# Performance work log

Hardware: AMD Instinct MI355X
Metric: run time of the kernel (lower is better)

The kernel has to match this reference:

```python
import jax, jax.numpy as jnp
import numpy as np

# Kronecker-sparse patterns (a,b,c,d), rightmost factor first, matching KSLinear.
PATTERNS = ((1, 64, 64, 64), (64, 64, 64, 1))
IN_SIZE = PATTERNS[0][0] * PATTERNS[0][2] * PATTERNS[0][3]   # 4096
OUT_SIZE = PATTERNS[-1][0] * PATTERNS[-1][1] * PATTERNS[-1][3]  # 4096
N_TOKENS = 16384


def setup_inputs() -> dict:
    key = jax.random.key(0)
    kx, k0, k1, kb = jax.random.split(key, 4)
    x = jax.random.normal(kx, (N_TOKENS, IN_SIZE), dtype=jnp.float32)
    # factors stored in native 4D (a,b,c,d) layout, uniform(-1/sqrt(c), 1/sqrt(c))
    a, b, c, d = PATTERNS[0]
    s0 = 1.0 / np.sqrt(c)
    f0 = jax.random.uniform(k0, (a, b, c, d), jnp.float32, -s0, s0)
    a, b, c, d = PATTERNS[1]
    s1 = 1.0 / np.sqrt(c)
    f1 = jax.random.uniform(k1, (a, b, c, d), jnp.float32, -s1, s1)
    bound = 1.0 / np.sqrt(IN_SIZE)
    bias = jax.random.uniform(kb, (OUT_SIZE,), jnp.float32, -bound, bound)
    return {"x": x, "f0": f0, "f1": f1, "bias": bias}


def _ks_apply(x, factor, pattern):
    # Apply one Kronecker-sparse factor with support I_a (x) 1_{b,c} (x) I_d.
    a, b, c, d = pattern
    batch = x.shape[:-1]
    x = x.reshape(*batch, a, c, d)                      # (..., a, c, d)
    y = jnp.einsum('...acd,abcd->...abd', x, factor)    # contract over c
    return y.reshape(*batch, a * b * d)


def reference(x, f0, f1, bias):
    y = _ks_apply(x, f0, PATTERNS[0])
    y = _ks_apply(y, f1, PATTERNS[1])
    return y + bias
```

## Files before the change

### kernel.cpp

```cpp
#include <hip/hip_runtime.h>
#include <cstdint>
#include <cstddef>

#define DI __device__ __forceinline__

using f32x4  = __attribute__((ext_vector_type(4))) float;
using bf16x8 = __attribute__((ext_vector_type(8))) short;
using u32x2  = __attribute__((ext_vector_type(2))) unsigned int;
using u32x4  = __attribute__((ext_vector_type(4))) unsigned int;

constexpr int NT = 16384;
constexpr int NF = 4096;

DI unsigned short f2bf(float f) {
  union { float f; unsigned u; } v; v.f = f;
  unsigned u = v.u;
  u += 0x7fffu + ((u >> 16) & 1u);
  return (unsigned short)(u >> 16);
}

__global__ void ks_prep(const float* __restrict__ f0, const float* __restrict__ f1,
                        unsigned short* __restrict__ f0s, unsigned short* __restrict__ f1s) {
  int tid = blockIdx.x * 256 + threadIdx.x;
  if (tid < 262144) {
    int d = tid & 63, c = (tid >> 6) & 63, b = tid >> 12;
    f0s[d * 4096 + b * 64 + c] = f2bf(f0[tid]);
  } else {
    int t2 = tid - 262144;
    f1s[t2] = f2bf(f1[t2]);
  }
}

__global__ __launch_bounds__(512, 4) void ks1(
    const float* __restrict__ x, const unsigned short* __restrict__ f0s,
    unsigned short* __restrict__ yp)
{
  __shared__ __align__(16) char L[32768 + 2 * 16640];
  char* const Xb0 = L;
  char* const Xb1 = L + 16384;
  char* const Yb0 = L + 32768;
  char* const Yb1 = L + 32768 + 16640;

  const int w  = blockIdx.x;
  const int tt = (w & 7) | ((w >> 6) << 3);
  const int dg = (w >> 3) & 7;
  const long T0 = (long)tt * 128;

  const int tid = threadIdx.x, lane = tid & 63, wv = tid >> 6;
  const int l15 = lane & 15, lq = lane >> 4;
  const int d = dg * 8 + wv;

  bf16x8 fA[4][2];
  #pragma unroll
  for (int bt = 0; bt < 4; ++bt)
    #pragma unroll
    for (int kh = 0; kh < 2; ++kh)
      fA[bt][kh] = *(const bf16x8*)(f0s + (size_t)d * 4096 + (bt * 16 + l15) * 64 + kh * 32 + lq * 8);

  const int st_t = tid >> 5, st_c0 = (tid >> 1) & 15, st_dq = tid & 1;
  const float* const xrow0 = x + (T0 + st_t) * (long)NF + dg * 8 + st_dq * 4;
  const int wkey = (st_t & 7) << 4;

  f32x4 r0, r1, r2, r3;
  auto issue = [&](int st) {
    const float* p = xrow0 + (long)st * 16 * NF + st_c0 * 4 * 64;
    r0 = *(const f32x4*)(p);
    r1 = *(const f32x4*)(p + 64);
    r2 = *(const f32x4*)(p + 128);
    r3 = *(const f32x4*)(p + 192);
  };
  auto stageX = [&](char* X) {
    #pragma unroll
    for (int e = 0; e < 4; ++e) {
      int p = st_dq * 4 + e;
      unsigned lo = (unsigned)f2bf(r0[e]) | ((unsigned)f2bf(r1[e]) << 16);
      unsigned hi = (unsigned)f2bf(r2[e]) | ((unsigned)f2bf(r3[e]) << 16);
      *(u32x2*)(X + p * 2048 + st_t * 128 + ((st_c0 * 8) ^ wkey)) = u32x2{lo, hi};
    }
  };

  issue(0);
  stageX(Xb0);
  issue(1);
  __syncthreads();

  const int rkey = (l15 & 7) << 4;

  for (int st = 0; st < 8; ++st) {
    char* const Xc = (st & 1) ? Xb1 : Xb0;
    char* const Xn = (st & 1) ? Xb0 : Xb1;
    char* const Yc = (st & 1) ? Yb1 : Yb0;

    const char* Xs = Xc + wv * 2048 + l15 * 128;
    bf16x8 bx0 = *(const bf16x8*)(Xs + ((0  + lq * 16) ^ rkey));
    bf16x8 bx1 = *(const bf16x8*)(Xs + ((64 + lq * 16) ^ rkey));
    f32x4 acc[4];
    #pragma unroll
    for (int bt = 0; bt < 4; ++bt) {
      acc[bt] = __builtin_amdgcn_mfma_f32_16x16x32_bf16(fA[bt][0], bx0, (f32x4){0.f,0.f,0.f,0.f}, 0, 0, 0);
      acc[bt] = __builtin_amdgcn_mfma_f32_16x16x32_bf16(fA[bt][1], bx1, acc[bt], 0, 0, 0);
    }

    {
      char* Yw = Yc + l15 * 1040 + wv * 2;
      #pragma unroll
      for (int bt = 0; bt < 4; ++bt)
        #pragma unroll
        for (int i = 0; i < 4; ++i)
          *(unsigned short*)(Yw + (bt * 16 + lq * 4 + i) * 16) = f2bf(acc[bt][i]);
    }

    stageX(Xn);
    issue(st + 2 <= 7 ? st + 2 : 7);
    __syncthreads();

    {
      const char* Yr = Yc;
      #pragma unroll
      for (int h = 0; h < 2; ++h) {
        int t = (tid >> 6) + h * 8;
        int c16 = tid & 63;
        u32x4 v = *(const u32x4*)(Yr + t * 1040 + c16 * 16);
        *(u32x4*)(yp + (T0 + st * 16 + t) * (size_t)NF + dg * 512 + c16 * 8) = v;
      }
    }
  }
}

__global__ __launch_bounds__(512, 4) void ks2(
    const unsigned short* __restrict__ yp, const unsigned short* __restrict__ f1s,
    const float* __restrict__ bias, float* __restrict__ out)
{
  const int bid = blockIdx.x;
  const int ag  = bid & 7;
  const long T0 = (long)(bid >> 3) * 128;

  const int tid = threadIdx.x, lane = tid & 63, wv = tid >> 6;
  const int l15 = lane & 15, lq = lane >> 4;
  const int a = ag * 8 + wv;

  bf16x8 fa[4][2];
  #pragma unroll
  for (int bt = 0; bt < 4; ++bt)
    #pragma unroll
    for (int kh = 0; kh < 2; ++kh)
      fa[bt][kh] = *(const bf16x8*)(f1s + (size_t)a * 4096 + (bt * 16 + l15) * 64 + kh * 32 + lq * 8);
  f32x4 bv[4];
  #pragma unroll
  for (int bt = 0; bt < 4; ++bt)
    bv[bt] = *(const f32x4*)(bias + a * 64 + bt * 16 + lq * 4);

  const unsigned short* const yb = yp + (T0 + l15) * (size_t)NF + lq * 512 + a * 8;
  float* const ob = out + (T0 + l15) * (size_t)NF + a * 64 + lq * 4;

  bf16x8 c0 = *(const bf16x8*)(yb);
  bf16x8 c1 = *(const bf16x8*)(yb + 2048);
  bf16x8 p0 = *(const bf16x8*)(yb + 65536);
  bf16x8 p1 = *(const bf16x8*)(yb + 65536 + 2048);

  #pragma unroll
  for (int t8 = 0; t8 < 8; ++t8) {
    bf16x8 q0 = p0, q1 = p1;
    if (t8 < 6) {
      q0 = *(const bf16x8*)(yb + (t8 + 2) * 65536);
      q1 = *(const bf16x8*)(yb + (t8 + 2) * 65536 + 2048);
    }
    f32x4 acc[4];
    #pragma unroll
    for (int bt = 0; bt < 4; ++bt) {
      acc[bt] = __builtin_amdgcn_mfma_f32_16x16x32_bf16(fa[bt][0], c0, (f32x4){0.f,0.f,0.f,0.f}, 0, 0, 0);
      acc[bt] = __builtin_amdgcn_mfma_f32_16x16x32_bf16(fa[bt][1], c1, acc[bt], 0, 0, 0);
    }
    float* op = ob + (size_t)t8 * 16 * NF;
    #pragma unroll
    for (int bt = 0; bt < 4; ++bt)
      *(f32x4*)(op + bt * 16) = acc[bt] + bv[bt];
    c0 = p0; c1 = p1;
    p0 = q0; p1 = q1;
  }
}

__global__ void ks_naive(const float* __restrict__ x, const float* __restrict__ f0,
                         const float* __restrict__ f1, const float* __restrict__ bias,
                         float* __restrict__ out)
{
  __shared__ float xr[4096];
  __shared__ float yr[4096];
  long t = blockIdx.x;
  int tid = threadIdx.x;
  for (int i = tid; i < 4096; i += 256) xr[i] = x[t * 4096 + i];
  __syncthreads();
  for (int i = tid; i < 4096; i += 256) {
    int b = i >> 6, d = i & 63;
    float s = 0.f;
    for (int c = 0; c < 64; ++c) s += xr[c * 64 + d] * f0[(b * 64 + c) * 64 + d];
    yr[i] = s;
  }
  __syncthreads();
  for (int i = tid; i < 4096; i += 256) {
    int a = i >> 6;
    float s = bias[i];
    for (int c = 0; c < 64; ++c) s += yr[a * 64 + c] * f1[(size_t)i * 64 + c];
    out[t * 4096 + i] = s;
  }
}

extern "C" void kernel_launch(void* const* d_in, const int* in_sizes, int n_in,
                              void* d_out, int out_size, void* d_ws, size_t ws_size,
                              hipStream_t stream) {
  const float* x    = (const float*)d_in[0];
  const float* f0   = (const float*)d_in[1];
  const float* f1   = (const float*)d_in[2];
  const float* bias = (const float*)d_in[3];
  float* out = (float*)d_out;

  const size_t ybytes = (size_t)NT * NF * 2;
  const size_t fbytes = (size_t)64 * 64 * 64 * 2;
  if (ws_size >= ybytes + 2 * fbytes) {
    unsigned short* yw  = (unsigned short*)d_ws;
    unsigned short* f0s = yw + (size_t)NT * NF;
    unsigned short* f1s = f0s + 64 * 64 * 64;
    ks_prep<<<2048, 256, 0, stream>>>(f0, f1, f0s, f1s);
    ks1<<<1024, 512, 0, stream>>>(x, f0s, yw);
    ks2<<<1024, 512, 0, stream>>>(yw, f1s, bias, out);
  } else {
    ks_naive<<<NT, 256, 0, stream>>>(x, f0, f1, bias, out);
  }
}
```

Measured before the change: 238.9 us.

## Stage ks2 input tiles into LDS via async global_load_lds double buffering

The second-stage kernel now copies 32-token tiles of the bf16 intermediate into a double-buffered, XOR-swizzled LDS buffer with direct global-to-LDS loads, then reads MFMA operands from LDS. Each block covers 256 tokens instead of 128, so the grid is halved. The aim is wider, coalesced 128-byte global reads instead of scattered 16-byte per-lane loads, with the next tile's load overlapping the current compute and stores. In exchange it adds 64KB of LDS per block, which limits occupancy. It also relies on a hand-written vmcnt wait count that depends on the number of stores issued in between.

```diff
diff --git a/kernel.cpp b/kernel.cpp
--- a/kernel.cpp
+++ b/kernel.cpp
@@ -17,6 +17,12 @@
   unsigned u = v.u;
   u += 0x7fffu + ((u >> 16) & 1u);
   return (unsigned short)(u >> 16);
+}
+
+DI void gload_lds16(const void* g, void* l) {
+  __builtin_amdgcn_global_load_lds(
+      (const __attribute__((address_space(1))) unsigned int*)g,
+      (__attribute__((address_space(3))) unsigned int*)l, 16, 0, 0);
 }
 
 __global__ void ks_prep(const float* __restrict__ f0, const float* __restrict__ f1,
@@ -131,9 +137,11 @@
     const unsigned short* __restrict__ yp, const unsigned short* __restrict__ f1s,
     const float* __restrict__ bias, float* __restrict__ out)
 {
+  __shared__ __align__(16) char Yb[2][32768];
+
   const int bid = blockIdx.x;
   const int ag  = bid & 7;
-  const long T0 = (long)(bid >> 3) * 128;
+  const long T0 = (long)(bid >> 3) * 256;
 
   const int tid = threadIdx.x, lane = tid & 63, wv = tid >> 6;
   const int l15 = lane & 15, lq = lane >> 4;
@@ -150,33 +158,46 @@
   for (int bt = 0; bt < 4; ++bt)
     bv[bt] = *(const f32x4*)(bias + a * 64 + bt * 16 + lq * 4);
 
-  const unsigned short* const yb = yp + (T0 + l15) * (size_t)NF + lq * 512 + a * 8;
-  float* const ob = out + (T0 + l15) * (size_t)NF + a * 64 + lq * 4;
-
-  bf16x8 c0 = *(const bf16x8*)(yb);
-  bf16x8 c1 = *(const bf16x8*)(yb + 2048);
-  bf16x8 p0 = *(const bf16x8*)(yb + 65536);
-  bf16x8 p1 = *(const bf16x8*)(yb + 65536 + 2048);
-
-  #pragma unroll
-  for (int t8 = 0; t8 < 8; ++t8) {
-    bf16x8 q0 = p0, q1 = p1;
-    if (t8 < 6) {
-      q0 = *(const bf16x8*)(yb + (t8 + 2) * 65536);
-      q1 = *(const bf16x8*)(yb + (t8 + 2) * 65536 + 2048);
-    }
-    f32x4 acc[4];
-    #pragma unroll
-    for (int bt = 0; bt < 4; ++bt) {
-      acc[bt] = __builtin_amdgcn_mfma_f32_16x16x32_bf16(fa[bt][0], c0, (f32x4){0.f,0.f,0.f,0.f}, 0, 0, 0);
-      acc[bt] = __builtin_amdgcn_mfma_f32_16x16x32_bf16(fa[bt][1], c1, acc[bt], 0, 0, 0);
-    }
-    float* op = ob + (size_t)t8 * 16 * NF;
-    #pragma unroll
-    for (int bt = 0; bt < 4; ++bt)
-      *(f32x4*)(op + bt * 16) = acc[bt] + bv[bt];
-    c0 = p0; c1 = p1;
-    p0 = q0; p1 = q1;
+  auto stage = [&](int tile, int buf) {
+    #pragma unroll
+    for (int i = 0; i < 4; ++i) {
+      const int trow = i * 8 + wv;
+      const int g = lane ^ (trow & 7);
+      const char* src = (const char*)yp + (T0 + (long)tile * 32 + trow) * 8192
+                        + ((g >> 3) << 10) + ag * 128 + (g & 7) * 16;
+      gload_lds16(src, &Yb[buf][trow * 1024]);
+    }
+  };
+
+  stage(0, 0);
+  asm volatile("s_waitcnt vmcnt(0)" ::: "memory");
+  __syncthreads();
+
+  #pragma unroll
+  for (int tile = 0; tile < 8; ++tile) {
+    if (tile < 7) stage(tile + 1, (tile + 1) & 1);
+
+    const char* Yt = Yb[tile & 1];
+    const int sw = wv ^ (l15 & 7);
+    #pragma unroll
+    for (int tt = 0; tt < 2; ++tt) {
+      const char* Yr = Yt + (tt * 16 + l15) * 1024;
+      bf16x8 c0 = *(const bf16x8*)(Yr + ((lq * 8 + sw) * 16));
+      bf16x8 c1 = *(const bf16x8*)(Yr + (((4 + lq) * 8 + sw) * 16));
+      f32x4 acc[4];
+      #pragma unroll
+      for (int bt = 0; bt < 4; ++bt) {
+        acc[bt] = __builtin_amdgcn_mfma_f32_16x16x32_bf16(fa[bt][0], c0, (f32x4){0.f,0.f,0.f,0.f}, 0, 0, 0);
+        acc[bt] = __builtin_amdgcn_mfma_f32_16x16x32_bf16(fa[bt][1], c1, acc[bt], 0, 0, 0);
+      }
+      float* op = out + (T0 + (long)tile * 32 + tt * 16 + l15) * NF + a * 64 + lq * 4;
+      #pragma unroll
+      for (int bt = 0; bt < 4; ++bt)
+        *(f32x4*)(op + bt * 16) = acc[bt] + bv[bt];
+    }
+
+    asm volatile("s_waitcnt vmcnt(8)" ::: "memory");
+    __syncthreads();
   }
 }
 
@@ -222,7 +243,7 @@
     unsigned short* f1s = f0s + 64 * 64 * 64;
     ks_prep<<<2048, 256, 0, stream>>>(f0, f1, f0s, f1s);
     ks1<<<1024, 512, 0, stream>>>(x, f0s, yw);
-    ks2<<<1024, 512, 0, stream>>>(yw, f1s, bias, out);
+    ks2<<<512, 512, 0, stream>>>(yw, f1s, bias, out);
   } else {
     ks_naive<<<NT, 256, 0, stream>>>(x, f0, f1, bias, out);
   }
```

Result: faster. 206.9 us (-13.4%).

## Store intermediate in chunk-major layout so ks2 reads contiguous token runs

Applied to the files above, without the earlier changes.

Changes the bf16 intermediate buffer layout from token-major rows to a [b*8+d-group][token][8] layout, so ks2 reads 16-byte vectors contiguously across tokens. ks1's LDS transpose is redone to match: packed 8-byte stores into a padded Y tile, then gathering 8 scalar halfwords per thread to form each 16-byte global write. ks2's prefetch loop is restructured to two-deep pairwise loads. The aim is better coalescing for ks2's loads, at the cost of more scalar LDS reads and possible bank conflicts in ks1.

```diff
diff --git a/kernel.cpp b/kernel.cpp
--- a/kernel.cpp
+++ b/kernel.cpp
@@ -11,6 +11,7 @@
 
 constexpr int NT = 16384;
 constexpr int NF = 4096;
+
 
 DI unsigned short f2bf(float f) {
   union { float f; unsigned u; } v; v.f = f;
@@ -35,11 +36,11 @@
     const float* __restrict__ x, const unsigned short* __restrict__ f0s,
     unsigned short* __restrict__ yp)
 {
-  __shared__ __align__(16) char L[32768 + 2 * 16640];
+  __shared__ __align__(16) char L[32768 + 2 * 16704];
   char* const Xb0 = L;
   char* const Xb1 = L + 16384;
   char* const Yb0 = L + 32768;
-  char* const Yb1 = L + 32768 + 16640;
+  char* const Yb1 = L + 32768 + 16704;
 
   const int w  = blockIdx.x;
   const int tt = (w & 7) | ((w >> 6) << 3);
@@ -85,6 +86,7 @@
   __syncthreads();
 
   const int rkey = (l15 & 7) << 4;
+  const int ct = tid & 15, cb0 = tid >> 4;
 
   for (int st = 0; st < 8; ++st) {
     char* const Xc = (st & 1) ? Xb1 : Xb0;
@@ -102,27 +104,31 @@
     }
 
     {
-      char* Yw = Yc + l15 * 1040 + wv * 2;
+      char* Yw = Yc + l15 * 1044 + wv * 128 + lq * 8;
       #pragma unroll
-      for (int bt = 0; bt < 4; ++bt)
-        #pragma unroll
-        for (int i = 0; i < 4; ++i)
-          *(unsigned short*)(Yw + (bt * 16 + lq * 4 + i) * 16) = f2bf(acc[bt][i]);
+      for (int bt = 0; bt < 4; ++bt) {
+        unsigned lo = (unsigned)f2bf(acc[bt][0]) | ((unsigned)f2bf(acc[bt][1]) << 16);
+        unsigned hi = (unsigned)f2bf(acc[bt][2]) | ((unsigned)f2bf(acc[bt][3]) << 16);
+        *(u32x2*)(Yw + bt * 32) = u32x2{lo, hi};
+      }
     }
 
     stageX(Xn);
     issue(st + 2 <= 7 ? st + 2 : 7);
     __syncthreads();
 
-    {
-      const char* Yr = Yc;
+    #pragma unroll
+    for (int h = 0; h < 2; ++h) {
+      const int b = cb0 + h * 32;
+      const char* Ys = Yc + ct * 1044 + b * 2;
+      unsigned short hv[8];
       #pragma unroll
-      for (int h = 0; h < 2; ++h) {
-        int t = (tid >> 6) + h * 8;
-        int c16 = tid & 63;
-        u32x4 v = *(const u32x4*)(Yr + t * 1040 + c16 * 16);
-        *(u32x4*)(yp + (T0 + st * 16 + t) * (size_t)NF + dg * 512 + c16 * 8) = v;
-      }
+      for (int j = 0; j < 8; ++j) hv[j] = *(const unsigned short*)(Ys + j * 128);
+      u32x4 wq;
+      #pragma unroll
+      for (int m = 0; m < 4; ++m)
+        wq[m] = (unsigned)hv[2 * m] | ((unsigned)hv[2 * m + 1] << 16);
+      *(u32x4*)((char*)yp + ((size_t)(b * 8 + dg) * 16384 + (T0 + st * 16 + ct)) * 16) = wq;
     }
   }
 }
@@ -150,33 +156,42 @@
   for (int bt = 0; bt < 4; ++bt)
     bv[bt] = *(const f32x4*)(bias + a * 64 + bt * 16 + lq * 4);
 
-  const unsigned short* const yb = yp + (T0 + l15) * (size_t)NF + lq * 512 + a * 8;
+  const char* const yb = (const char*)yp + ((size_t)(a * 8 + lq) * 16384 + T0 + l15) * 16;
+  constexpr size_t KH1 = (size_t)4 * 16384 * 16;
   float* const ob = out + (T0 + l15) * (size_t)NF + a * 64 + lq * 4;
 
-  bf16x8 c0 = *(const bf16x8*)(yb);
-  bf16x8 c1 = *(const bf16x8*)(yb + 2048);
-  bf16x8 p0 = *(const bf16x8*)(yb + 65536);
-  bf16x8 p1 = *(const bf16x8*)(yb + 65536 + 2048);
-
-  #pragma unroll
-  for (int t8 = 0; t8 < 8; ++t8) {
-    bf16x8 q0 = p0, q1 = p1;
-    if (t8 < 6) {
-      q0 = *(const bf16x8*)(yb + (t8 + 2) * 65536);
-      q1 = *(const bf16x8*)(yb + (t8 + 2) * 65536 + 2048);
-    }
+  auto compute = [&](int j, bf16x8 c0, bf16x8 c1) {
     f32x4 acc[4];
     #pragma unroll
     for (int bt = 0; bt < 4; ++bt) {
       acc[bt] = __builtin_amdgcn_mfma_f32_16x16x32_bf16(fa[bt][0], c0, (f32x4){0.f,0.f,0.f,0.f}, 0, 0, 0);
       acc[bt] = __builtin_amdgcn_mfma_f32_16x16x32_bf16(fa[bt][1], c1, acc[bt], 0, 0, 0);
     }
-    float* op = ob + (size_t)t8 * 16 * NF;
+    float* op = ob + (size_t)j * 16 * NF;
     #pragma unroll
     for (int bt = 0; bt < 4; ++bt)
       *(f32x4*)(op + bt * 16) = acc[bt] + bv[bt];
-    c0 = p0; c1 = p1;
-    p0 = q0; p1 = q1;
+  };
+
+  bf16x8 A0 = *(const bf16x8*)(yb);
+  bf16x8 A1 = *(const bf16x8*)(yb + KH1);
+  bf16x8 B0 = *(const bf16x8*)(yb + 256);
+  bf16x8 B1 = *(const bf16x8*)(yb + KH1 + 256);
+
+  #pragma unroll
+  for (int j = 0; j < 8; j += 2) {
+    bf16x8 nA0 = A0, nA1 = A1, nB0 = B0, nB1 = B1;
+    if (j + 2 < 8) {
+      nA0 = *(const bf16x8*)(yb + (j + 2) * 256);
+      nA1 = *(const bf16x8*)(yb + KH1 + (j + 2) * 256);
+    }
+    compute(j, A0, A1);
+    if (j + 3 < 8) {
+      nB0 = *(const bf16x8*)(yb + (j + 3) * 256);
+      nB1 = *(const bf16x8*)(yb + KH1 + (j + 3) * 256);
+    }
+    compute(j + 1, B0, B1);
+    A0 = nA0; A1 = nA1; B0 = nB0; B1 = nB1;
   }
 }
 
```

Measured after the change: 206.3 us. 13.6% less time.
